# Kernel optimization log

Measured on AMD Instinct MI355X. Metric: run time of the kernel, lower is better.

## Reference

```python
import jax, jax.numpy as jnp
import numpy as np

N_NODES = 50000
N_EDGES = 600000
IN_FEAT = 128
OUT_FEAT = 128
NUM_RELS = 8


def setup_inputs() -> dict:
    key = jax.random.key(0)
    ks = jax.random.split(key, 8)
    h = jax.random.normal(ks[0], (N_NODES, IN_FEAT), dtype=jnp.float32)
    # xavier_uniform-like scale for relation weights
    limit = float(np.sqrt(6.0 / (IN_FEAT + OUT_FEAT)))
    weight = jax.random.uniform(ks[1], (NUM_RELS, IN_FEAT, OUT_FEAT), jnp.float32, -limit, limit)
    limit_g = float(np.sqrt(6.0 / (IN_FEAT + 1)))
    gate_weight = jax.random.uniform(ks[2], (NUM_RELS, IN_FEAT, 1), jnp.float32, -limit_g, limit_g)
    h_bias = jnp.zeros((OUT_FEAT,), jnp.float32)
    loop_weight = jax.random.uniform(ks[3], (IN_FEAT, OUT_FEAT), jnp.float32, -limit, limit)
    norm = jax.random.uniform(ks[4], (N_EDGES, 1), jnp.float32)
    src = jax.random.randint(ks[5], (N_EDGES,), 0, N_NODES, dtype=jnp.int32)
    dst = jax.random.randint(ks[6], (N_EDGES,), 0, N_NODES, dtype=jnp.int32)
    rel_type = jax.random.randint(ks[7], (N_EDGES,), 0, NUM_RELS, dtype=jnp.int32)
    return {"h": h, "weight": weight, "gate_weight": gate_weight, "h_bias": h_bias,
            "loop_weight": loop_weight, "norm": norm, "src": src, "dst": dst,
            "rel_type": rel_type}


def reference(h, weight, gate_weight, h_bias, loop_weight, norm, src, dst, rel_type):
    n_nodes = h.shape[0]
    # Transform all nodes under every relation once ([R, N, out]); cheaper than
    # materializing per-edge [E, in, out] weight gathers for small R.
    h_rel = jnp.einsum('ni,rio->rno', h, weight)          # [R, N, out]
    msg = h_rel[rel_type, src]                             # [E, out] gather
    msg = msg * norm                                       # per-edge norm
    # relation-specific scalar gate on src features
    gate_rel = jnp.einsum('ni,ri->rn', h, gate_weight[:, :, 0])  # [R, N]
    gate = jax.nn.sigmoid(gate_rel[rel_type, src])[:, None]      # [E, 1]
    msg = msg * gate
    # scatter-sum messages into destination nodes
    agg = jax.ops.segment_sum(msg, dst, num_segments=n_nodes)    # [N, out]
    out = agg + h_bias + h @ loop_weight                   # bias + self-loop
    out = jax.nn.relu(out)                                 # activation
    # dropout p=0.0 (deterministic) -> identity
    return out
```

## Files before the change

### kernel.cpp

```cpp
#include <hip/hip_runtime.h>

#define N_NODES 50000
#define N_EDGES 600000
#define F 128
#define NRELL 9
#define NB_SCAN 196
#define NB2 1563

#define WT3_OFF   0
#define H2_OFF    294912
#define GATE3_OFF 13094912
#define CNT3_OFF  14694912
#define EXCL3_OFF 16294912
#define BSUM3_OFF 17895168
#define REC3_OFF  17901568
#define A3_OFF    22701568
#define WS_NEED3  ((size_t)125199872)

#define GATE_OFF   294912
#define HREL_OFF   1894912
#define HREL_BYTES (9ll*N_NODES*128*2)
#define CNT_OFF    117094912
#define BASE_OFF   117294912
#define CUR_OFF    117494912
#define BSUM_OFF   117694912
#define SORT_OFF   117695936
#define WS_NEED2   ((size_t)120095936)
#define WS_NEED1   ((size_t)HREL_OFF + (size_t)HREL_BYTES)

typedef __attribute__((ext_vector_type(8))) short short8;
typedef __attribute__((ext_vector_type(4))) float floatx4;

__device__ inline unsigned short f32_to_bf16(float f) {
    unsigned u = __float_as_uint(f);
    unsigned r = u + 0x7fff + ((u >> 16) & 1);
    return (unsigned short)(r >> 16);
}
__device__ inline float bf16_to_f32(unsigned short s) {
    return __uint_as_float(((unsigned)s) << 16);
}
__device__ inline float bf16lo(unsigned m) { return __uint_as_float(m << 16); }
__device__ inline float bf16hi(unsigned m) { return __uint_as_float(m & 0xffff0000u); }
__device__ inline float sigmoidf(float x) { return 1.f / (1.f + __expf(-x)); }
__device__ inline unsigned packbf(float a0, float a1) {
    return (unsigned)f32_to_bf16(a0) | ((unsigned)f32_to_bf16(a1) << 16);
}

__global__ __launch_bounds__(256) void k_prep(
    const float* __restrict__ h, const float* __restrict__ W,
    const float* __restrict__ gw, const float* __restrict__ lw,
    const int* __restrict__ dst, const int* __restrict__ rel,
    unsigned short* __restrict__ Wt, unsigned short* __restrict__ h2,
    float* __restrict__ gate, int* __restrict__ cnt)
{
    int vb = blockIdx.x, tid = threadIdx.x;
    if (vb < 576) {
        int idx = vb * 256 + tid;
        int r = idx >> 14, rem = idx & 16383, i = rem >> 7, o = rem & 127;
        float v = (r < 8) ? W[(r << 14) + (i << 7) + o] : lw[(i << 7) + o];
        int g = (i >> 3) ^ (o & 7);
        Wt[(r << 14) + (o << 7) + (g << 3) + (i & 7)] = f32_to_bf16(v);
    } else if (vb < 13076) {
        int wave = tid >> 6, lane = tid & 63;
        int n = (vb - 576) * 4 + wave;
        float2 hv = *(const float2*)(h + (size_t)n * F + lane * 2);
        *(unsigned*)(h2 + (size_t)n * F + lane * 2) = packbf(hv.x, hv.y);
        float g = 0.f;
        #pragma unroll
        for (int r = 0; r < 8; ++r) {
            float2 wv = *(const float2*)(gw + r * F + lane * 2);
            float p = hv.x * wv.x + hv.y * wv.y;
            #pragma unroll
            for (int off = 32; off; off >>= 1) p += __shfl_xor(p, off);
            if (lane == r) g = sigmoidf(p);
        }
        if (lane < 8) gate[(size_t)n * 8 + lane] = g;
    } else {
        int e = (vb - 13076) * 256 + tid;
        if (e < N_EDGES) atomicAdd(&cnt[dst[e] * 8 + rel[e]], 1);
    }
}

__global__ void k_s1(const int* __restrict__ cnt, int* __restrict__ excl,
                     int* __restrict__ bsum) {
    __shared__ int sh[256];
    int g = blockIdx.x * 256 + threadIdx.x;
    int v = (g < 400000) ? cnt[g] : 0;
    sh[threadIdx.x] = v;
    __syncthreads();
    #pragma unroll
    for (int off = 1; off < 256; off <<= 1) {
        int t = (threadIdx.x >= off) ? sh[threadIdx.x - off] : 0;
        __syncthreads();
        sh[threadIdx.x] += t;
        __syncthreads();
    }
    if (g < 400000) excl[g] = sh[threadIdx.x] - v;
    if (threadIdx.x == 255) bsum[blockIdx.x] = sh[255];
}

__global__ void k_s2(int* __restrict__ bsum) {
    __shared__ int sh[256];
    int t = threadIdx.x;
    int v[7];
    int s = 0;
    #pragma unroll
    for (int j = 0; j < 7; ++j) {
        int idx = t * 7 + j;
        v[j] = (idx < NB2) ? bsum[idx] : 0;
        s += v[j];
    }
    sh[t] = s;
    __syncthreads();
    #pragma unroll
    for (int off = 1; off < 256; off <<= 1) {
        int tt = (t >= off) ? sh[t - off] : 0;
        __syncthreads();
        sh[t] += tt;
        __syncthreads();
    }
    int run = sh[t] - s;
    #pragma unroll
    for (int j = 0; j < 7; ++j) {
        int idx = t * 7 + j;
        if (idx < NB2) bsum[idx] = run;
        run += v[j];
    }
}

__global__ void k_s3(int* __restrict__ excl, const int* __restrict__ bsum,
                     int* __restrict__ cursor) {
    int g = blockIdx.x * 256 + threadIdx.x;
    if (g < 400000) {
        int b = excl[g] + bsum[blockIdx.x];
        excl[g] = b;
        cursor[g] = b;
    }
    if (g == 0) excl[400000] = N_EDGES;
}

__global__ void k_scatter2(const int* __restrict__ src, const int* __restrict__ dst,
                           const int* __restrict__ rel, const float* __restrict__ norm,
                           const float* __restrict__ gate, int* __restrict__ cursor,
                           int2* __restrict__ rec) {
    int e = blockIdx.x * 256 + threadIdx.x;
    if (e >= N_EDGES) return;
    int d = dst[e], r = rel[e], s = src[e];
    int pos = atomicAdd(&cursor[d * 8 + r], 1);
    float sc = norm[e] * gate[(size_t)s * 8 + r];
    rec[pos] = make_int2(s, __float_as_int(sc));
}

__global__ __launch_bounds__(256) void k_aggA(const unsigned short* __restrict__ h2,
                                              const int2* __restrict__ rec,
                                              const int* __restrict__ excl,
                                              unsigned short* __restrict__ A) {
    int wave = threadIdx.x >> 6, lane = threadIdx.x & 63;
    int n = blockIdx.x * 4 + wave;
    int ex = 0;
    if (lane < 9) ex = excl[n * 8 + lane];
    int e0 = __shfl(ex, 0), e8 = __shfl(ex, 8);
    int deg = e8 - e0;
    unsigned short* Arow = A + (size_t)n * 1024;
    int swo = (((lane >> 2) ^ (n & 7)) << 2) + (lane & 3);

    if (deg <= 64) {
        int rs = 0; float rsc = 0.f;
        if (lane < deg) {
            int2 rc = rec[e0 + lane];
            rs = rc.x; rsc = __int_as_float(rc.y);
        }
        for (int r = 0; r < 8; ++r) {
            int s = __shfl(ex, r) - e0;
            int e = __shfl(ex, r + 1) - e0;
            float a0 = 0.f, a1 = 0.f;
            for (int j = s; j < e; ++j) {
                int sj = __shfl(rs, j);
                float sc = __shfl(rsc, j);
                unsigned m = *(const unsigned*)(h2 + (size_t)sj * F + lane * 2);
                a0 += sc * bf16lo(m);
                a1 += sc * bf16hi(m);
            }
            ((unsigned*)(Arow + r * 128))[swo] = packbf(a0, a1);
        }
    } else {
        for (int r = 0; r < 8; ++r) {
            int s = __shfl(ex, r);
            int e = __shfl(ex, r + 1);
            float a0 = 0.f, a1 = 0.f;
            for (int idx = s; idx < e; ++idx) {
                int2 rc = rec[idx];
                float sc = __int_as_float(rc.y);
                unsigned m = *(const unsigned*)(h2 + (size_t)rc.x * F + lane * 2);
                a0 += sc * bf16lo(m);
                a1 += sc * bf16hi(m);
            }
            ((unsigned*)(Arow + r * 128))[swo] = packbf(a0, a1);
        }
    }
}

__global__ __launch_bounds__(256) void k_gemmA(const unsigned short* __restrict__ A,
                                               const unsigned short* __restrict__ h2,
                                               const unsigned short* __restrict__ Wt,
                                               const float* __restrict__ bias,
                                               float* __restrict__ out) {
    __shared__ unsigned short sA[16384];
    __shared__ unsigned short sB[16384];
    int tid = threadIdx.x;
    int nb = blockIdx.x * 128;
    int wave = tid >> 6, lane = tid & 63, lrow = lane & 15, quad = lane >> 4;

    floatx4 acc[2][8];
    #pragma unroll
    for (int mt = 0; mt < 2; ++mt)
        #pragma unroll
        for (int nt = 0; nt < 8; ++nt) acc[mt][nt] = (floatx4){0.f, 0.f, 0.f, 0.f};

    for (int kb = 0; kb < 9; ++kb) {
        __syncthreads();
        if (kb < 8) {
            #pragma unroll
            for (int it = 0; it < 8; ++it) {
                int g = it * 256 + tid;
                int row = g >> 4, gr = g & 15;
                *(uint4*)(&sA[row * 128 + gr * 8]) =
                    *(const uint4*)(A + (size_t)(nb + row) * 1024 + kb * 128 + gr * 8);
                *(uint4*)(&sB[row * 128 + gr * 8]) =
                    *(const uint4*)(Wt + (kb << 14) + (g << 3));
            }
        } else {
            #pragma unroll
            for (int it = 0; it < 8; ++it) {
                int g = it * 256 + tid;
                int row = g >> 4, gr = g & 15;
                *(uint4*)(&sA[row * 128 + (gr ^ (row & 7)) * 8]) =
                    *(const uint4*)(h2 + (size_t)(nb + row) * F + gr * 8);
                *(uint4*)(&sB[row * 128 + gr * 8]) =
                    *(const uint4*)(Wt + (kb << 14) + (g << 3));
            }
        }
        __syncthreads();
        #pragma unroll
        for (int kt = 0; kt < 4; ++kt) {
            int j = kt * 4 + quad;
            int sw = (j ^ (lrow & 7)) << 3;
            short8 a0 = *(const short8*)(&sA[(wave * 32 + lrow) * 128 + sw]);
            short8 a1 = *(const short8*)(&sA[(wave * 32 + 16 + lrow) * 128 + sw]);
            #pragma unroll
            for (int nt = 0; nt < 8; ++nt) {
                short8 b = *(const short8*)(&sB[(nt * 16 + lrow) * 128 + sw]);
                acc[0][nt] = __builtin_amdgcn_mfma_f32_16x16x32_bf16(a0, b, acc[0][nt], 0, 0, 0);
                acc[1][nt] = __builtin_amdgcn_mfma_f32_16x16x32_bf16(a1, b, acc[1][nt], 0, 0, 0);
            }
        }
    }
    #pragma unroll
    for (int mt = 0; mt < 2; ++mt) {
        #pragma unroll
        for (int nt = 0; nt < 8; ++nt) {
            int col = nt * 16 + lrow;
            float bv = bias[col];
            #pragma unroll
            for (int g = 0; g < 4; ++g) {
                int row = nb + wave * 32 + mt * 16 + quad * 4 + g;
                if (row < N_NODES)
                    out[(size_t)row * F + col] = fmaxf(acc[mt][nt][g] + bv, 0.f);
            }
        }
    }
}

__global__ void k_prep_w(const float* __restrict__ W, const float* __restrict__ LW,
                         unsigned short* __restrict__ Wt, int swz) {
    int idx = blockIdx.x * 256 + threadIdx.x;
    if (idx >= 9 * 128 * 128) return;
    int r = idx >> 14;
    int rem = idx & 16383;
    int i = rem >> 7, o = rem & 127;
    float v = (r < 8) ? W[(r << 14) + (i << 7) + o] : LW[(i << 7) + o];
    int pos;
    if (swz) {
        int g = (i >> 3) ^ (o & 7);
        pos = (r << 14) + (o << 7) + (g << 3) + (i & 7);
    } else {
        pos = (r << 14) + (o << 7) + i;
    }
    Wt[pos] = f32_to_bf16(v);
}

__global__ void k_gate(const float* __restrict__ h, const float* __restrict__ gw,
                       float* __restrict__ gate) {
    int wave = threadIdx.x >> 6, lane = threadIdx.x & 63;
    int n = blockIdx.x * 4 + wave;
    if (n >= N_NODES) return;
    float2 hv = *(const float2*)(h + (size_t)n * F + lane * 2);
    #pragma unroll
    for (int r = 0; r < 8; ++r) {
        float2 wv = *(const float2*)(gw + r * F + lane * 2);
        float p = hv.x * wv.x + hv.y * wv.y;
        #pragma unroll
        for (int off = 32; off; off >>= 1) p += __shfl_xor(p, off);
        if (lane == 0) gate[r * N_NODES + n] = sigmoidf(p);
    }
}

#define LDH 136
#define LDW 136
__global__ __launch_bounds__(256) void k_hrel(const float* __restrict__ h,
                                              const unsigned short* __restrict__ Wt,
                                              unsigned short* __restrict__ hrel) {
    __shared__ unsigned short hA[64 * LDH];
    __shared__ unsigned short wB[128 * LDW];
    int tid = threadIdx.x;
    int nb = blockIdx.x * 64;
    #pragma unroll
    for (int it = 0; it < 8; ++it) {
        int idx = it * 1024 + tid * 4;
        int row = idx >> 7, col = idx & 127;
        int node = nb + row;
        float4 v;
        if (node < N_NODES) v = *(const float4*)(h + (size_t)node * F + col);
        else                v = make_float4(0.f, 0.f, 0.f, 0.f);
        ushort4 b;
        b.x = f32_to_bf16(v.x); b.y = f32_to_bf16(v.y);
        b.z = f32_to_bf16(v.z); b.w = f32_to_bf16(v.w);
        *(ushort4*)(&hA[row * LDH + col]) = b;
    }
    int wave = tid >> 6, lane = tid & 63;
    int lrow = lane & 15, quad = lane >> 4;
    const unsigned short* aptr = &hA[(wave * 16 + lrow) * LDH + quad * 8];
    for (int r = 0; r < NRELL; ++r) {
        __syncthreads();
        #pragma unroll
        for (int it = 0; it < 8; ++it) {
            int idx = it * 2048 + tid * 8;
            int o = idx >> 7, i = idx & 127;
            *(uint4*)(&wB[o * LDW + i]) = *(const uint4*)(Wt + (r << 14) + idx);
        }
        __syncthreads();
        floatx4 acc[8];
        #pragma unroll
        for (int nt = 0; nt < 8; ++nt) acc[nt] = (floatx4){0.f, 0.f, 0.f, 0.f};
        #pragma unroll
        for (int kt = 0; kt < 4; ++kt) {
            short8 a = *(const short8*)(aptr + kt * 32);
            #pragma unroll
            for (int nt = 0; nt < 8; ++nt) {
                short8 b = *(const short8*)(&wB[(nt * 16 + lrow) * LDW + kt * 32 + quad * 8]);
                acc[nt] = __builtin_amdgcn_mfma_f32_16x16x32_bf16(a, b, acc[nt], 0, 0, 0);
            }
        }
        unsigned short* dstp = hrel + (size_t)r * N_NODES * F;
        #pragma unroll
        for (int nt = 0; nt < 8; ++nt) {
            #pragma unroll
            for (int g = 0; g < 4; ++g) {
                int node = nb + wave * 16 + quad * 4 + g;
                if (node < N_NODES)
                    dstp[(size_t)node * F + nt * 16 + lrow] = f32_to_bf16(acc[nt][g]);
            }
        }
    }
}

__global__ void k_hist(const int* __restrict__ dst, int* __restrict__ cnt) {
    int e = blockIdx.x * 256 + threadIdx.x;
    if (e < N_EDGES) atomicAdd(&cnt[dst[e]], 1);
}

__global__ void k_scan1(const int* __restrict__ cnt, int* __restrict__ excl,
                        int* __restrict__ bsum) {
    __shared__ int sh[256];
    int g = blockIdx.x * 256 + threadIdx.x;
    int v = (g < N_NODES) ? cnt[g] : 0;
    sh[threadIdx.x] = v;
    __syncthreads();
    #pragma unroll
    for (int off = 1; off < 256; off <<= 1) {
        int t = (threadIdx.x >= off) ? sh[threadIdx.x - off] : 0;
        __syncthreads();
        sh[threadIdx.x] += t;
        __syncthreads();
    }
    if (g < N_NODES) excl[g] = sh[threadIdx.x] - v;
    if (threadIdx.x == 255) bsum[blockIdx.x] = sh[255];
}

__global__ void k_scan2(int* __restrict__ bsum) {
    __shared__ int sh[256];
    int v = (threadIdx.x < NB_SCAN) ? bsum[threadIdx.x] : 0;
    sh[threadIdx.x] = v;
    __syncthreads();
    #pragma unroll
    for (int off = 1; off < 256; off <<= 1) {
        int t = (threadIdx.x >= off) ? sh[threadIdx.x - off] : 0;
        __syncthreads();
        sh[threadIdx.x] += t;
        __syncthreads();
    }
    if (threadIdx.x < NB_SCAN) bsum[threadIdx.x] = sh[threadIdx.x] - v;
}

__global__ void k_scan3(int* __restrict__ excl, const int* __restrict__ bsum,
                        int* __restrict__ cursor) {
    int g = blockIdx.x * 256 + threadIdx.x;
    if (g < N_NODES) {
        int b = excl[g] + bsum[blockIdx.x];
        excl[g] = b;
        cursor[g] = b;
    }
}

__global__ void k_scatter(const int* __restrict__ dst, int* __restrict__ cursor,
                          int* __restrict__ sorted) {
    int e = blockIdx.x * 256 + threadIdx.x;
    if (e < N_EDGES) {
        int pos = atomicAdd(&cursor[dst[e]], 1);
        sorted[pos] = e;
    }
}

__global__ __launch_bounds__(256) void k_agg(const unsigned short* __restrict__ hrel,
                      const float* __restrict__ gate,
                      const float* __restrict__ norm,
                      const int* __restrict__ src, const int* __restrict__ rel,
                      const int* __restrict__ sorted,
                      const int* __restrict__ base, const int* __restrict__ cnt,
                      const float* __restrict__ bias,
                      float* __restrict__ out) {
    int wave = threadIdx.x >> 6, lane = threadIdx.x & 63;
    int n = blockIdx.x * 4 + wave;
    if (n >= N_NODES) return;
    int startp = base[n];
    int deg = cnt[n];
    float acc0 = 0.f, acc1 = 0.f;
    for (int c0 = 0; c0 < deg; c0 += 64) {
        int myi = c0 + lane;
        float sc = 0.f;
        int row = 0;
        if (myi < deg) {
            int e = sorted[startp + myi];
            int s = src[e], r = rel[e];
            row = r * N_NODES + s;
            sc = norm[e] * gate[row];
        }
        int lim = (deg - c0 < 64) ? (deg - c0) : 64;
        for (int i = 0; i < lim; ++i) {
            float scl = __shfl(sc, i);
            int rw = __shfl(row, i);
            unsigned m = *(const unsigned*)(hrel + (size_t)rw * F + lane * 2);
            acc0 += scl * bf16lo(m);
            acc1 += scl * bf16hi(m);
        }
    }
    const unsigned short* hrel8 = hrel + (size_t)8 * N_NODES * F;
    unsigned l8 = *(const unsigned*)(hrel8 + (size_t)n * F + lane * 2);
    float2 bv = *(const float2*)(bias + lane * 2);
    float o0 = fmaxf(acc0 + bv.x + bf16lo(l8), 0.f);
    float o1 = fmaxf(acc1 + bv.y + bf16hi(l8), 0.f);
    *(float2*)(out + (size_t)n * F + lane * 2) = make_float2(o0, o1);
}

__global__ void k_edges(const unsigned short* __restrict__ hrel,
                        const float* __restrict__ gate,
                        const float* __restrict__ norm,
                        const int* __restrict__ src, const int* __restrict__ dst,
                        const int* __restrict__ rel,
                        float* __restrict__ out) {
    int wave = threadIdx.x >> 6, lane = threadIdx.x & 63;
    int e = blockIdx.x * 4 + wave;
    if (e >= N_EDGES) return;
    int s = src[e], d = dst[e], r = rel[e];
    float scale = norm[e] * gate[r * N_NODES + s];
    unsigned int m = *(const unsigned int*)(hrel + ((size_t)r * N_NODES + s) * F + lane * 2);
    float v0 = bf16lo(m) * scale;
    float v1 = bf16hi(m) * scale;
    float* op = out + (size_t)d * F + lane * 2;
    unsafeAtomicAdd(op, v0);
    unsafeAtomicAdd(op + 1, v1);
}

__global__ void k_final(float* __restrict__ out, const float* __restrict__ bias,
                        const unsigned short* __restrict__ hrel8) {
    int idx = blockIdx.x * 256 + threadIdx.x;
    if (idx >= N_NODES * 32) return;
    int node = idx >> 5, c4 = (idx & 31) * 4;
    float4 a = *(float4*)(out + (size_t)node * F + c4);
    float4 b = *(const float4*)(bias + c4);
    ushort4 l = *(const ushort4*)(hrel8 + (size_t)node * F + c4);
    float o0 = fmaxf(a.x + b.x + bf16_to_f32(l.x), 0.f);
    float o1 = fmaxf(a.y + b.y + bf16_to_f32(l.y), 0.f);
    float o2 = fmaxf(a.z + b.z + bf16_to_f32(l.z), 0.f);
    float o3 = fmaxf(a.w + b.w + bf16_to_f32(l.w), 0.f);
    *(float4*)(out + (size_t)node * F + c4) = make_float4(o0, o1, o2, o3);
}

__global__ void k_edges_fb(const float* __restrict__ h, const float* __restrict__ W,
                           const float* __restrict__ gw, const float* __restrict__ norm,
                           const int* __restrict__ src, const int* __restrict__ dst,
                           const int* __restrict__ rel, float* __restrict__ out) {
    int wave = threadIdx.x >> 6, lane = threadIdx.x & 63;
    int e = blockIdx.x * 4 + wave;
    if (e >= N_EDGES) return;
    int s = src[e], d = dst[e], r = rel[e];
    float2 hv = *(const float2*)(h + (size_t)s * F + lane * 2);
    float2 gv = *(const float2*)(gw + r * F + lane * 2);
    float p = hv.x * gv.x + hv.y * gv.y;
    #pragma unroll
    for (int off = 32; off; off >>= 1) p += __shfl_xor(p, off);
    float scale = norm[e] * sigmoidf(p);
    const float* wr = W + ((size_t)r << 14);
    float a0 = 0.f, a1 = 0.f;
    for (int i2 = 0; i2 < 64; ++i2) {
        float x0 = __shfl(hv.x, i2), x1 = __shfl(hv.y, i2);
        a0 += x0 * wr[(2 * i2) * F + lane]      + x1 * wr[(2 * i2 + 1) * F + lane];
        a1 += x0 * wr[(2 * i2) * F + 64 + lane] + x1 * wr[(2 * i2 + 1) * F + 64 + lane];
    }
    unsafeAtomicAdd(out + (size_t)d * F + lane,      a0 * scale);
    unsafeAtomicAdd(out + (size_t)d * F + 64 + lane, a1 * scale);
}

__global__ void k_final_fb(const float* __restrict__ h, const float* __restrict__ LW,
                           const float* __restrict__ bias, float* __restrict__ out) {
    int wave = threadIdx.x >> 6, lane = threadIdx.x & 63;
    int n = blockIdx.x * 4 + wave;
    if (n >= N_NODES) return;
    float2 hv = *(const float2*)(h + (size_t)n * F + lane * 2);
    float a0 = 0.f, a1 = 0.f;
    for (int i2 = 0; i2 < 64; ++i2) {
        float x0 = __shfl(hv.x, i2), x1 = __shfl(hv.y, i2);
        a0 += x0 * LW[(2 * i2) * F + lane]      + x1 * LW[(2 * i2 + 1) * F + lane];
        a1 += x0 * LW[(2 * i2) * F + 64 + lane] + x1 * LW[(2 * i2 + 1) * F + 64 + lane];
    }
    float* op = out + (size_t)n * F;
    op[lane]      = fmaxf(op[lane]      + bias[lane]      + a0, 0.f);
    op[64 + lane] = fmaxf(op[64 + lane] + bias[64 + lane] + a1, 0.f);
}

extern "C" void kernel_launch(void* const* d_in, const int* in_sizes, int n_in,
                              void* d_out, int out_size, void* d_ws, size_t ws_size,
                              hipStream_t stream) {
    const float* h    = (const float*)d_in[0];
    const float* W    = (const float*)d_in[1];
    const float* gw   = (const float*)d_in[2];
    const float* bias = (const float*)d_in[3];
    const float* lw   = (const float*)d_in[4];
    const float* norm = (const float*)d_in[5];
    const int* src    = (const int*)d_in[6];
    const int* dst    = (const int*)d_in[7];
    const int* rel    = (const int*)d_in[8];
    float* out = (float*)d_out;

    if (ws_size >= WS_NEED3) {
        unsigned short* Wt   = (unsigned short*)((char*)d_ws + WT3_OFF);
        unsigned short* h2   = (unsigned short*)((char*)d_ws + H2_OFF);
        float*          gate = (float*)((char*)d_ws + GATE3_OFF);
        int*            cnt  = (int*)((char*)d_ws + CNT3_OFF);
        int*            excl = (int*)((char*)d_ws + EXCL3_OFF);
        int*            bsum = (int*)((char*)d_ws + BSUM3_OFF);
        int2*           rec  = (int2*)((char*)d_ws + REC3_OFF);
        unsigned short* A    = (unsigned short*)((char*)d_ws + A3_OFF);

        hipMemsetAsync(cnt, 0, 400000 * sizeof(int), stream);
        k_prep<<<15420, 256, 0, stream>>>(h, W, gw, lw, dst, rel, Wt, h2, gate, cnt);
        k_s1<<<NB2, 256, 0, stream>>>(cnt, excl, bsum);
        k_s2<<<1, 256, 0, stream>>>(bsum);
        k_s3<<<NB2, 256, 0, stream>>>(excl, bsum, cnt);
        k_scatter2<<<2344, 256, 0, stream>>>(src, dst, rel, norm, gate, cnt, rec);
        k_aggA<<<12500, 256, 0, stream>>>(h2, rec, excl, A);
        k_gemmA<<<391, 256, 0, stream>>>(A, h2, Wt, bias, out);
    } else if (ws_size >= WS_NEED2) {
        unsigned short* Wt   = (unsigned short*)d_ws;
        float*          gate = (float*)((char*)d_ws + GATE_OFF);
        unsigned short* hrel = (unsigned short*)((char*)d_ws + HREL_OFF);
        int* cnt    = (int*)((char*)d_ws + CNT_OFF);
        int* base   = (int*)((char*)d_ws + BASE_OFF);
        int* cursor = (int*)((char*)d_ws + CUR_OFF);
        int* bsum   = (int*)((char*)d_ws + BSUM_OFF);
        int* sorted = (int*)((char*)d_ws + SORT_OFF);
        hipMemsetAsync(cnt, 0, N_NODES * sizeof(int), stream);
        k_prep_w<<<576, 256, 0, stream>>>(W, lw, Wt, 0);
        k_gate<<<12500, 256, 0, stream>>>(h, gw, gate);
        k_hist<<<2344, 256, 0, stream>>>(dst, cnt);
        k_scan1<<<NB_SCAN, 256, 0, stream>>>(cnt, base, bsum);
        k_scan2<<<1, 256, 0, stream>>>(bsum);
        k_scan3<<<NB_SCAN, 256, 0, stream>>>(base, bsum, cursor);
        k_scatter<<<2344, 256, 0, stream>>>(dst, cursor, sorted);
        k_hrel<<<782, 256, 0, stream>>>(h, Wt, hrel);
        k_agg<<<12500, 256, 0, stream>>>(hrel, gate, norm, src, rel, sorted,
                                         base, cnt, bias, out);
    } else if (ws_size >= WS_NEED1) {
        unsigned short* Wt   = (unsigned short*)d_ws;
        float*          gate = (float*)((char*)d_ws + GATE_OFF);
        unsigned short* hrel = (unsigned short*)((char*)d_ws + HREL_OFF);
        hipMemsetAsync(d_out, 0, (size_t)out_size * sizeof(float), stream);
        k_prep_w<<<576, 256, 0, stream>>>(W, lw, Wt, 0);
        k_gate<<<12500, 256, 0, stream>>>(h, gw, gate);
        k_hrel<<<782, 256, 0, stream>>>(h, Wt, hrel);
        k_edges<<<150000, 256, 0, stream>>>(hrel, gate, norm, src, dst, rel, out);
        k_final<<<6250, 256, 0, stream>>>(out, bias, hrel + (size_t)8 * N_NODES * F);
    } else {
        hipMemsetAsync(d_out, 0, (size_t)out_size * sizeof(float), stream);
        k_edges_fb<<<150000, 256, 0, stream>>>(h, W, gw, norm, src, dst, rel, out);
        k_final_fb<<<12500, 256, 0, stream>>>(h, lw, bias, out);
    }
}
```

Measured before the change: 284.0 us.

## Load GEMM A operand straight to registers, stream weights via global_load_lds, halve tile

The final GEMM now reads its A fragments directly from global memory into registers instead of staging them through shared memory. Weight tiles are copied into LDS with the direct global-to-LDS load builtin, and the block tile shrinks to 64 rows across a 2x2 wave grid, so twice as many blocks launch. The gate computation in the prep kernel is also reworked so each lane group handles one relation with float4 loads, needing three shuffles instead of eight full reductions. The aim is higher occupancy, less LDS traffic and lower prep cost, at the price of every block re-fetching the full weight matrix and less B reuse per block.

```diff
diff --git a/kernel.cpp b/kernel.cpp
--- a/kernel.cpp
+++ b/kernel.cpp
@@ -44,6 +44,12 @@
 __device__ inline float sigmoidf(float x) { return 1.f / (1.f + __expf(-x)); }
 __device__ inline unsigned packbf(float a0, float a1) {
     return (unsigned)f32_to_bf16(a0) | ((unsigned)f32_to_bf16(a1) << 16);
+}
+
+__device__ __forceinline__ void gload_lds16(const void* gsrc, void* ldst) {
+    __builtin_amdgcn_global_load_lds(
+        (const __attribute__((address_space(1))) void*)gsrc,
+        (__attribute__((address_space(3))) void*)ldst, 16, 0, 0);
 }
 
 __global__ __launch_bounds__(256) void k_prep(
@@ -65,16 +71,19 @@
         int n = (vb - 576) * 4 + wave;
         float2 hv = *(const float2*)(h + (size_t)n * F + lane * 2);
         *(unsigned*)(h2 + (size_t)n * F + lane * 2) = packbf(hv.x, hv.y);
-        float g = 0.f;
-        #pragma unroll
-        for (int r = 0; r < 8; ++r) {
-            float2 wv = *(const float2*)(gw + r * F + lane * 2);
-            float p = hv.x * wv.x + hv.y * wv.y;
-            #pragma unroll
-            for (int off = 32; off; off >>= 1) p += __shfl_xor(p, off);
-            if (lane == r) g = sigmoidf(p);
-        }
-        if (lane < 8) gate[(size_t)n * 8 + lane] = g;
+        int rl = lane >> 3, seg = lane & 7;
+        const float4* hp = (const float4*)(h + (size_t)n * F + seg * 16);
+        const float4* wp = (const float4*)(gw + rl * F + seg * 16);
+        float p = 0.f;
+        #pragma unroll
+        for (int j = 0; j < 4; ++j) {
+            float4 a = hp[j], b = wp[j];
+            p += a.x * b.x + a.y * b.y + a.z * b.z + a.w * b.w;
+        }
+        p += __shfl_xor(p, 1);
+        p += __shfl_xor(p, 2);
+        p += __shfl_xor(p, 4);
+        if (seg == 0) gate[(size_t)n * 8 + rl] = sigmoidf(p);
     } else {
         int e = (vb - 13076) * 256 + tid;
         if (e < N_EDGES) atomicAdd(&cnt[dst[e] * 8 + rel[e]], 1);
@@ -205,65 +214,69 @@
                                                const unsigned short* __restrict__ Wt,
                                                const float* __restrict__ bias,
                                                float* __restrict__ out) {
-    __shared__ unsigned short sA[16384];
     __shared__ unsigned short sB[16384];
     int tid = threadIdx.x;
-    int nb = blockIdx.x * 128;
+    int nb = blockIdx.x * 64;
     int wave = tid >> 6, lane = tid & 63, lrow = lane & 15, quad = lane >> 4;
-
-    floatx4 acc[2][8];
+    int wr = wave >> 1, wc = wave & 1;
+
+    floatx4 acc[2][4];
     #pragma unroll
     for (int mt = 0; mt < 2; ++mt)
         #pragma unroll
-        for (int nt = 0; nt < 8; ++nt) acc[mt][nt] = (floatx4){0.f, 0.f, 0.f, 0.f};
+        for (int nt = 0; nt < 4; ++nt) acc[mt][nt] = (floatx4){0.f, 0.f, 0.f, 0.f};
+
+    const unsigned short* Ar0 = A + (size_t)(nb + wr * 32 + lrow) * 1024;
+    const unsigned short* Ar1 = Ar0 + (size_t)16 * 1024;
+    const unsigned short* Hr0 = h2 + (size_t)(nb + wr * 32 + lrow) * F;
+    const unsigned short* Hr1 = Hr0 + (size_t)16 * F;
+    int sk = lrow & 7;
 
     for (int kb = 0; kb < 9; ++kb) {
-        __syncthreads();
+        short8 a0r[4], a1r[4];
         if (kb < 8) {
             #pragma unroll
-            for (int it = 0; it < 8; ++it) {
-                int g = it * 256 + tid;
-                int row = g >> 4, gr = g & 15;
-                *(uint4*)(&sA[row * 128 + gr * 8]) =
-                    *(const uint4*)(A + (size_t)(nb + row) * 1024 + kb * 128 + gr * 8);
-                *(uint4*)(&sB[row * 128 + gr * 8]) =
-                    *(const uint4*)(Wt + (kb << 14) + (g << 3));
+            for (int kt = 0; kt < 4; ++kt) {
+                int gphys = ((kt * 4 + quad) ^ sk) << 3;
+                a0r[kt] = *(const short8*)(Ar0 + kb * 128 + gphys);
+                a1r[kt] = *(const short8*)(Ar1 + kb * 128 + gphys);
             }
         } else {
             #pragma unroll
-            for (int it = 0; it < 8; ++it) {
-                int g = it * 256 + tid;
-                int row = g >> 4, gr = g & 15;
-                *(uint4*)(&sA[row * 128 + (gr ^ (row & 7)) * 8]) =
-                    *(const uint4*)(h2 + (size_t)(nb + row) * F + gr * 8);
-                *(uint4*)(&sB[row * 128 + gr * 8]) =
-                    *(const uint4*)(Wt + (kb << 14) + (g << 3));
-            }
+            for (int kt = 0; kt < 4; ++kt) {
+                int goff = (kt * 4 + quad) << 3;
+                a0r[kt] = *(const short8*)(Hr0 + goff);
+                a1r[kt] = *(const short8*)(Hr1 + goff);
+            }
+        }
+        __syncthreads();
+        #pragma unroll
+        for (int it = 0; it < 8; ++it) {
+            int c = it * 4 + wave;
+            gload_lds16((const char*)Wt + (kb << 15) + (c << 10) + lane * 16,
+                        (char*)sB + (c << 10));
         }
         __syncthreads();
         #pragma unroll
         for (int kt = 0; kt < 4; ++kt) {
-            int j = kt * 4 + quad;
-            int sw = (j ^ (lrow & 7)) << 3;
-            short8 a0 = *(const short8*)(&sA[(wave * 32 + lrow) * 128 + sw]);
-            short8 a1 = *(const short8*)(&sA[(wave * 32 + 16 + lrow) * 128 + sw]);
+            int gphys = ((kt * 4 + quad) ^ sk) << 3;
             #pragma unroll
-            for (int nt = 0; nt < 8; ++nt) {
-                short8 b = *(const short8*)(&sB[(nt * 16 + lrow) * 128 + sw]);
-                acc[0][nt] = __builtin_amdgcn_mfma_f32_16x16x32_bf16(a0, b, acc[0][nt], 0, 0, 0);
-                acc[1][nt] = __builtin_amdgcn_mfma_f32_16x16x32_bf16(a1, b, acc[1][nt], 0, 0, 0);
+            for (int nt = 0; nt < 4; ++nt) {
+                short8 b = *(const short8*)(&sB[(wc * 64 + nt * 16 + lrow) * 128 + gphys]);
+                acc[0][nt] = __builtin_amdgcn_mfma_f32_16x16x32_bf16(a0r[kt], b, acc[0][nt], 0, 0, 0);
+                acc[1][nt] = __builtin_amdgcn_mfma_f32_16x16x32_bf16(a1r[kt], b, acc[1][nt], 0, 0, 0);
             }
         }
     }
     #pragma unroll
     for (int mt = 0; mt < 2; ++mt) {
         #pragma unroll
-        for (int nt = 0; nt < 8; ++nt) {
-            int col = nt * 16 + lrow;
+        for (int nt = 0; nt < 4; ++nt) {
+            int col = wc * 64 + nt * 16 + lrow;
             float bv = bias[col];
             #pragma unroll
             for (int g = 0; g < 4; ++g) {
-                int row = nb + wave * 32 + mt * 16 + quad * 4 + g;
+                int row = nb + wr * 32 + mt * 16 + quad * 4 + g;
                 if (row < N_NODES)
                     out[(size_t)row * F + col] = fmaxf(acc[mt][nt][g] + bv, 0.f);
             }
@@ -569,7 +582,7 @@
         k_s3<<<NB2, 256, 0, stream>>>(excl, bsum, cnt);
         k_scatter2<<<2344, 256, 0, stream>>>(src, dst, rel, norm, gate, cnt, rec);
         k_aggA<<<12500, 256, 0, stream>>>(h2, rec, excl, A);
-        k_gemmA<<<391, 256, 0, stream>>>(A, h2, Wt, bias, out);
+        k_gemmA<<<782, 256, 0, stream>>>(A, h2, Wt, bias, out);
     } else if (ws_size >= WS_NEED2) {
         unsigned short* Wt   = (unsigned short*)d_ws;
         float*          gate = (float*)((char*)d_ws + GATE_OFF);
```

Measured after the change: 269.9 us. 5.0% less time.
